# Kernel optimization log

Hardware: AMD Instinct MI355X
Metric: run time of the kernel (lower is better)

The kernel has to match this reference:

```python
import jax, jax.numpy as jnp
import numpy as np

LAM = 0.43
IN_DIM = 256
BATCH = 512


def _persistence_pairs(D):
    """0-dim persistence pairs via Kruskal-style union-find (matches torch code).
    D: [n, n] numpy distance matrix. Returns [n-1, 2] int array of MST edges."""
    n = D.shape[0]
    parent = np.arange(n)

    def find(u):
        root = u
        while parent[root] != root:
            root = parent[root]
        while parent[u] != root:  # path compression
            parent[u], u = root, parent[u]
        return root

    iu, ju = np.triu_indices(n)  # includes diagonal, like triu_indices_from
    w = D[iu, ju]
    order = np.argsort(w, kind='stable')
    pairs = []
    for e in order:
        u, v = int(iu[e]), int(ju[e])
        ru, rv = find(u), find(v)
        if ru == rv:
            continue
        if ru > rv:
            parent[rv] = ru  # merge(v, u)
        else:
            parent[ru] = rv  # merge(u, v)
        pairs.append((u, v) if u < v else (v, u))
    return np.asarray(pairs, dtype=np.int64)  # exactly n-1 edges


def _pdist(x):
    # torch.norm(x[:, None] - x, dim=2, p=2)
    return jnp.linalg.norm(x[:, None, :] - x[None, :, :], axis=-1)


def setup_inputs() -> dict:
    key = jax.random.key(0)
    ks = jax.random.split(key, 16)
    d = IN_DIM
    dims = [(d, d // 2), (d // 2, d // 4), (d // 4, 2), (2, d // 4), (d // 4, d // 2), (d // 2, d)]
    inp = {
        'x': jax.random.normal(ks[0], (BATCH, d), dtype=jnp.float32),
        'label': jax.random.randint(ks[1], (BATCH,), 0, 10),
    }
    names = ['1', '2', 'm', '3', '4', '5']
    for i, (nm, (din, dout)) in enumerate(zip(names, dims)):
        s = 1.0 / np.sqrt(din)
        inp['W' + nm] = jax.random.uniform(ks[2 + 2 * i], (din, dout), minval=-s, maxval=s, dtype=jnp.float32)
        inp['b' + nm] = jax.random.uniform(ks[3 + 2 * i], (dout,), minval=-s, maxval=s, dtype=jnp.float32)
    inp['latent_norm'] = jnp.ones((1,), dtype=jnp.float32)
    return inp


def reference(x, label, W1, b1, W2, b2, Wm, bm, W3, b3, W4, b4, W5, b5, latent_norm):
    # Encoder
    h1 = jax.nn.relu(x @ W1 + b1)
    h2 = jax.nn.relu(h1 @ W2 + b2)
    lat = h2 @ Wm + bm  # [B, 2]

    # normalized pairwise distance matrices
    xd = _pdist(x)
    xd = xd / xd.max()  # 2D-input branch
    ld = _pdist(lat) / latent_norm[0]

    # Decoder
    h3 = jax.nn.relu(lat @ W3 + b3)
    h4 = jax.nn.relu(h3 @ W4 + b4)
    xr = h4 @ W5 + b5
    ae_loss = jnp.mean((x - xr) ** 2)

    # persistence pairs (detached / host computation, as in the torch code)
    p1 = _persistence_pairs(np.asarray(jax.device_get(xd)))
    p2 = _persistence_pairs(np.asarray(jax.device_get(ld)))

    sig1 = xd[p1[:, 0], p1[:, 1]]
    sig1_2 = ld[p1[:, 0], p1[:, 1]]
    sig2 = ld[p2[:, 0], p2[:, 1]]
    sig2_1 = xd[p2[:, 0], p2[:, 1]]
    topo = jnp.sum((sig1 - sig1_2) ** 2) + jnp.sum((sig2 - sig2_1) ** 2)

    loss = ae_loss + LAM * topo / float(x.shape[0])
    return loss
```

## Files before the change

kernel.cpp:

```cpp
#include <hip/hip_runtime.h>
#include <math.h>

#define N      512
#define DIN    256
#define LAM    0.43f
#define MAGIC  0x4D535431u
#define PAD(j) ((j) + (((j) >> 6) << 2))

#define OFF_LDREADY 4
#define OFF_T0READY 5
#define OFF_T0BITS  6
#define OFF_BLKMAX  8
#define OFF_AEPART  128
#define OFF_LAT     1024
#define OFF_XD      2048
#define OFF_LD      (2048 + 262144)
#define OFF_CAND    526336
#define OFF_BAR     (OFF_CAND + 18432)

__device__ __forceinline__ unsigned ld_acq(unsigned* p) {
    return __hip_atomic_load(p, __ATOMIC_ACQUIRE, __HIP_MEMORY_SCOPE_AGENT);
}
__device__ __forceinline__ void st_rel(unsigned* p, unsigned v) {
    __hip_atomic_store(p, v, __ATOMIC_RELEASE, __HIP_MEMORY_SCOPE_AGENT);
}
__device__ __forceinline__ unsigned ld_rlx(unsigned* p) {
    return __hip_atomic_load(p, __ATOMIC_RELAXED, __HIP_MEMORY_SCOPE_AGENT);
}
__device__ __forceinline__ unsigned long long ld64_rlx(unsigned long long* p) {
    return __hip_atomic_load(p, __ATOMIC_RELAXED, __HIP_MEMORY_SCOPE_AGENT);
}
__device__ __forceinline__ void st64_rlx(unsigned long long* p, unsigned long long v) {
    __hip_atomic_store(p, v, __ATOMIC_RELAXED, __HIP_MEMORY_SCOPE_AGENT);
}
__device__ __forceinline__ void spin_magic(unsigned* p) {
    while (ld_acq(p) != MAGIC) __builtin_amdgcn_s_sleep(1);
}

__global__ __launch_bounds__(256) void fused_mlp_pdistx_kernel(
    const float* __restrict__ x,
    const float* __restrict__ W1, const float* __restrict__ b1,
    const float* __restrict__ W2, const float* __restrict__ b2,
    const float* __restrict__ Wm, const float* __restrict__ bm,
    const float* __restrict__ W3, const float* __restrict__ b3,
    const float* __restrict__ W4, const float* __restrict__ b4,
    const float* __restrict__ W5, const float* __restrict__ b5,
    float* __restrict__ lat_out, float* __restrict__ ae_part,
    float* __restrict__ xd, float* __restrict__ blkmax)
{
    const int tid = threadIdx.x;

    if (blockIdx.x < 512) {
        __shared__ float xs[256];
        __shared__ float h1[128];
        __shared__ float h2[64];
        __shared__ float latv[2];
        __shared__ float h3[64];
        __shared__ float h4[128];
        __shared__ float red[4];

        const int row = blockIdx.x;
        xs[tid] = x[(size_t)row * DIN + tid];
        __syncthreads();

        if (tid < 128) {
            float s = b1[tid];
            for (int k = 0; k < 256; ++k) s = fmaf(xs[k], W1[k * 128 + tid], s);
            h1[tid] = fmaxf(s, 0.f);
        }
        __syncthreads();

        if (tid < 64) {
            float s = b2[tid];
            for (int k = 0; k < 128; ++k) s = fmaf(h1[k], W2[k * 64 + tid], s);
            h2[tid] = fmaxf(s, 0.f);
        }
        __syncthreads();

        if (tid < 2) {
            float s = bm[tid];
            for (int k = 0; k < 64; ++k) s = fmaf(h2[k], Wm[k * 2 + tid], s);
            latv[tid] = s;
            lat_out[(size_t)row * 2 + tid] = s;
        }
        __syncthreads();

        if (tid < 64) {
            float s = b3[tid];
            s = fmaf(latv[0], W3[tid], s);
            s = fmaf(latv[1], W3[64 + tid], s);
            h3[tid] = fmaxf(s, 0.f);
        }
        __syncthreads();

        if (tid < 128) {
            float s = b4[tid];
            for (int k = 0; k < 64; ++k) s = fmaf(h3[k], W4[k * 128 + tid], s);
            h4[tid] = fmaxf(s, 0.f);
        }
        __syncthreads();

        float s = b5[tid];
        for (int k = 0; k < 128; ++k) s = fmaf(h4[k], W5[k * 256 + tid], s);
        float diff = xs[tid] - s;
        float a = diff * diff;

        #pragma unroll
        for (int m = 1; m < 64; m <<= 1) a += __shfl_xor(a, m, 64);
        if ((tid & 63) == 0) red[tid >> 6] = a;
        __syncthreads();
        if (tid == 0) ae_part[row] = red[0] + red[1] + red[2] + red[3];
    } else {
        __shared__ float As[32][65];
        __shared__ float Bs[32][65];
        __shared__ float red2[4];

        const int bid = blockIdx.x - 512;
        const int bi = bid & 7, bj = bid >> 3;
        const int i0 = bi * 64, j0 = bj * 64;
        const int ty = tid >> 4, tx = tid & 15;

        float acc[4][4];
        #pragma unroll
        for (int i = 0; i < 4; ++i)
            #pragma unroll
            for (int j = 0; j < 4; ++j) acc[i][j] = 0.f;

        for (int kk = 0; kk < DIN; kk += 32) {
            #pragma unroll
            for (int s = tid; s < 512; s += 256) {
                int r = s >> 3, c4 = (s & 7) << 2;
                float4 va = *(const float4*)(x + (size_t)(i0 + r) * DIN + kk + c4);
                As[c4 + 0][r] = va.x; As[c4 + 1][r] = va.y;
                As[c4 + 2][r] = va.z; As[c4 + 3][r] = va.w;
                float4 vb = *(const float4*)(x + (size_t)(j0 + r) * DIN + kk + c4);
                Bs[c4 + 0][r] = vb.x; Bs[c4 + 1][r] = vb.y;
                Bs[c4 + 2][r] = vb.z; Bs[c4 + 3][r] = vb.w;
            }
            __syncthreads();
            #pragma unroll 8
            for (int k = 0; k < 32; ++k) {
                float a[4], b[4];
                #pragma unroll
                for (int i = 0; i < 4; ++i) a[i] = As[k][ty + 16 * i];
                #pragma unroll
                for (int j = 0; j < 4; ++j) b[j] = Bs[k][tx + 16 * j];
                #pragma unroll
                for (int i = 0; i < 4; ++i)
                    #pragma unroll
                    for (int j = 0; j < 4; ++j) {
                        float d = a[i] - b[j];
                        acc[i][j] = fmaf(d, d, acc[i][j]);
                    }
            }
            __syncthreads();
        }

        float lmax = 0.f;
        #pragma unroll
        for (int i = 0; i < 4; ++i)
            #pragma unroll
            for (int j = 0; j < 4; ++j) {
                float dd = sqrtf(acc[i][j]);
                int r = i0 + ty + 16 * i, c = j0 + tx + 16 * j;
                xd[(size_t)r * N + c] = dd;
                lmax = fmaxf(lmax, dd);
            }

        #pragma unroll
        for (int m = 32; m >= 1; m >>= 1) lmax = fmaxf(lmax, __shfl_xor(lmax, m, 64));
        if ((tid & 63) == 0) red2[tid >> 6] = lmax;
        __syncthreads();
        if (tid == 0)
            blkmax[bid] = fmaxf(fmaxf(red2[0], red2[1]), fmaxf(red2[2], red2[3]));
    }
}

__global__ __launch_bounds__(256) void mst_boruvka_kernel(
    const float* __restrict__ xd, float* __restrict__ ld,
    const float* __restrict__ lat, const float* __restrict__ latent_norm,
    const float* __restrict__ blkmax, const float* __restrict__ ae_part,
    float* __restrict__ wsf, float* __restrict__ out)
{
    __shared__ unsigned comp_a[512];
    __shared__ __align__(16) unsigned comp_s[544];
    __shared__ unsigned long long cval[512];
    __shared__ int tgt[512];
    __shared__ unsigned short eu[512], ev[512];
    __shared__ float ew[512];
    __shared__ float latx[512], laty[512];
    __shared__ float s_red[4];
    __shared__ float s_xdm;
    __shared__ int s_ecnt;

    const int tid = threadIdx.x;
    const int blk = blockIdx.x;
    const int m   = blk >> 6;
    const int wb  = blk & 63;
    const bool leader = (wb == 0);

    unsigned* ldready = (unsigned*)(wsf + OFF_LDREADY);
    unsigned* t0ready = (unsigned*)(wsf + OFF_T0READY);
    unsigned* t0bits  = (unsigned*)(wsf + OFF_T0BITS);
    unsigned long long* candm =
        (unsigned long long*)(wsf + OFF_CAND) + (size_t)m * 9 * 512;
    unsigned* bar = (unsigned*)(wsf + OFF_BAR) + (size_t)m * 640;

    const float* Dm = m ? ld : xd;
    const float* Om = m ? xd : ld;

    if (m == 1) {
        for (int i = tid; i < 512; i += 256) {
            latx[i] = lat[2 * i + 0];
            laty[i] = lat[2 * i + 1];
        }
        __syncthreads();
        const int r0 = wb << 3;
        for (int q = tid; q < 1024; q += 256) {
            int rr = r0 + (q >> 7);
            int j  = (q & 127) << 2;
            float xi = latx[rr], yi = laty[rr];
            float dx0 = xi - latx[j + 0], dy0 = yi - laty[j + 0];
            float dx1 = xi - latx[j + 1], dy1 = yi - laty[j + 1];
            float dx2 = xi - latx[j + 2], dy2 = yi - laty[j + 2];
            float dx3 = xi - latx[j + 3], dy3 = yi - laty[j + 3];
            float4 o;
            o.x = sqrtf(fmaf(dx0, dx0, dy0 * dy0));
            o.y = sqrtf(fmaf(dx1, dx1, dy1 * dy1));
            o.z = sqrtf(fmaf(dx2, dx2, dy2 * dy2));
            o.w = sqrtf(fmaf(dx3, dx3, dy3 * dy3));
            *(float4*)(ld + (size_t)rr * N + j) = o;
        }
    }

    for (int i = tid; i < 72; i += 256)
        st64_rlx(&candm[(size_t)wb * 72 + i], ~0ULL);

    for (int i = tid; i < 512; i += 256) {
        comp_a[i] = (unsigned)i;
        comp_s[PAD(i)] = (unsigned)i;
    }
    if (tid == 0) s_ecnt = 0;

    __syncthreads();
    if (tid == 0) st_rel(&bar[wb], MAGIC);
    if (tid < 64) spin_magic(&bar[tid]);
    __syncthreads();
    if (m == 1 && leader && tid == 0) st_rel(ldready, MAGIC);

    int nc = 512;
    for (int p = 0; p < 9 && nc > 1; ++p) {
        unsigned long long* cand = candm + (size_t)p * 512;

        {
            const int r  = (wb << 3) + (tid >> 5);
            const int c0 = (tid & 31) << 4;
            const unsigned cv = comp_s[PAD(r)];
            const float4* rp = (const float4*)(Dm + (size_t)r * N + c0);
            unsigned long long bk = ~0ULL;
            #pragma unroll
            for (int c = 0; c < 4; ++c) {
                float4 f = rp[c];
                int jb = c0 + 4 * c;
                int4 cc = *(const int4*)&comp_s[PAD(jb)];
                unsigned long long k;
                k = ((unsigned long long)__float_as_uint(f.x) << 18)
                  | ((unsigned long long)r << 9) | (unsigned)(jb + 0);
                if ((unsigned)cc.x != cv && k < bk) bk = k;
                k = ((unsigned long long)__float_as_uint(f.y) << 18)
                  | ((unsigned long long)r << 9) | (unsigned)(jb + 1);
                if ((unsigned)cc.y != cv && k < bk) bk = k;
                k = ((unsigned long long)__float_as_uint(f.z) << 18)
                  | ((unsigned long long)r << 9) | (unsigned)(jb + 2);
                if ((unsigned)cc.z != cv && k < bk) bk = k;
                k = ((unsigned long long)__float_as_uint(f.w) << 18)
                  | ((unsigned long long)r << 9) | (unsigned)(jb + 3);
                if ((unsigned)cc.w != cv && k < bk) bk = k;
            }
            #pragma unroll
            for (int mm = 1; mm <= 16; mm <<= 1) {
                unsigned long long o = __shfl_xor(bk, mm, 64);
                if (o < bk) bk = o;
            }
            if ((tid & 31) == 0 && bk != ~0ULL)
                atomicMin(&cand[cv], bk);
        }

        __syncthreads();
        if (tid == 0) st_rel(&bar[(p + 1) * 64 + wb], MAGIC);
        if (tid < 64) spin_magic(&bar[(p + 1) * 64 + tid]);
        __syncthreads();

        for (int i = tid; i < 512; i += 256) cval[i] = ld64_rlx(&cand[i]);
        __syncthreads();
        for (int i = tid; i < 512; i += 256) {
            int t = -1;
            if (comp_a[i] == (unsigned)i && cval[i] != ~0ULL)
                t = (int)comp_a[cval[i] & 511];
            tgt[i] = t;
        }
        __syncthreads();
        for (int i = tid; i < 512; i += 256) {
            int s = tgt[i];
            if (s >= 0 && !(tgt[s] == i && i > s)) {
                comp_a[i] = (unsigned)s;
                int e = atomicAdd(&s_ecnt, 1);
                unsigned long long c = cval[i];
                eu[e] = (unsigned short)((c >> 9) & 511);
                ev[e] = (unsigned short)(c & 511);
                ew[e] = __uint_as_float((unsigned)(c >> 18));
            }
        }
        __syncthreads();
        for (int dd = 0; dd < 9; ++dd) {
            unsigned a = comp_a[comp_a[tid]];
            unsigned b = comp_a[comp_a[tid + 256]];
            __syncthreads();
            comp_a[tid] = a; comp_a[tid + 256] = b;
            __syncthreads();
        }
        for (int i = tid; i < 512; i += 256) comp_s[PAD(i)] = comp_a[i];
        nc = 512 - s_ecnt;
        __syncthreads();
    }

    if (!leader) return;

    if (tid < 64) {
        float mx = blkmax[tid];
        #pragma unroll
        for (int mm = 32; mm >= 1; mm >>= 1)
            mx = fmaxf(mx, __shfl_xor(mx, mm, 64));
        if (tid == 0) s_xdm = mx;
    }
    __syncthreads();
    const float xdm = s_xdm;
    const float lnv = latent_norm[0];
    const float sD = (m == 0) ? 1.f / xdm : 1.f / lnv;
    const float sO = (m == 0) ? 1.f / lnv : 1.f / xdm;

    if (m == 0) {
        if (tid == 0) spin_magic(ldready);
        __syncthreads();
    }

    const int ne = s_ecnt;
    float acc = 0.f;
    for (int i = tid; i < ne; i += 256) {
        float de = ew[i];
        float oe = Om[(size_t)eu[i] * N + ev[i]];
        float c = sD * de - sO * oe;
        acc = fmaf(c, c, acc);
    }
    #pragma unroll
    for (int mm = 32; mm >= 1; mm >>= 1) acc += __shfl_xor(acc, mm, 64);
    if ((tid & 63) == 0) s_red[tid >> 6] = acc;
    __syncthreads();

    if (m == 0) {
        if (tid == 0) {
            float t0 = s_red[0] + s_red[1] + s_red[2] + s_red[3];
            __hip_atomic_store(t0bits, __float_as_uint(t0), __ATOMIC_RELAXED,
                               __HIP_MEMORY_SCOPE_AGENT);
            st_rel(t0ready, MAGIC);
        }
    } else {
        float t1 = 0.f;
        if (tid == 0) t1 = s_red[0] + s_red[1] + s_red[2] + s_red[3];
        __syncthreads();
        float a = ae_part[tid] + ae_part[tid + 256];
        #pragma unroll
        for (int mm = 32; mm >= 1; mm >>= 1) a += __shfl_xor(a, mm, 64);
        if ((tid & 63) == 0) s_red[tid >> 6] = a;
        __syncthreads();
        if (tid == 0) {
            float ae = s_red[0] + s_red[1] + s_red[2] + s_red[3];
            spin_magic(t0ready);
            float t0 = __uint_as_float(ld_rlx(t0bits));
            out[0] = ae * (1.f / (float)(N * DIN))
                   + (LAM * (t0 + t1)) * (1.f / (float)N);
        }
    }
}

extern "C" void kernel_launch(void* const* d_in, const int* in_sizes, int n_in,
                              void* d_out, int out_size, void* d_ws, size_t ws_size,
                              hipStream_t stream) {
    const float* x   = (const float*)d_in[0];
    const float* W1  = (const float*)d_in[2];
    const float* b1  = (const float*)d_in[3];
    const float* W2  = (const float*)d_in[4];
    const float* b2  = (const float*)d_in[5];
    const float* Wm  = (const float*)d_in[6];
    const float* bm  = (const float*)d_in[7];
    const float* W3  = (const float*)d_in[8];
    const float* b3  = (const float*)d_in[9];
    const float* W4  = (const float*)d_in[10];
    const float* b4  = (const float*)d_in[11];
    const float* W5  = (const float*)d_in[12];
    const float* b5  = (const float*)d_in[13];
    const float* latent_norm = (const float*)d_in[14];

    float* ws      = (float*)d_ws;
    float* blkmax  = ws + OFF_BLKMAX;
    float* ae_part = ws + OFF_AEPART;
    float* lat     = ws + OFF_LAT;
    float* xd      = ws + OFF_XD;
    float* ld      = ws + OFF_LD;

    fused_mlp_pdistx_kernel<<<576, 256, 0, stream>>>(
        x, W1, b1, W2, b2, Wm, bm, W3, b3, W4, b4, W5, b5,
        lat, ae_part, xd, blkmax);
    mst_boruvka_kernel<<<128, 256, 0, stream>>>(
        xd, ld, lat, latent_norm, blkmax, ae_part, ws, (float*)d_out);
}
```

Baseline: 159.2 us.

## Merge MLP, pdist and Boruvka MST into one persistent 128-block kernel

Fuses both launches into a single 128-block kernel. Group 0 computes the x distance matrix and group 1 runs the autoencoder eight rows per block, with the weight loads reused across rows. Groups coordinate through global spin barriers instead of a kernel boundary. Distributed Boruvka rounds now stop once 64 components remain, after which a leader block finishes the MST on a 64x64 component table held in shared memory, trading global barriers for single-block work. This drops one launch and several cross-block barrier rounds, but adds more shared memory per block and relies on all 128 blocks being co-resident.

```diff
diff --git a/kernel.cpp b/kernel.cpp
--- a/kernel.cpp
+++ b/kernel.cpp
@@ -1,5 +1,7 @@
 #include <hip/hip_runtime.h>
 #include <math.h>
+
+typedef unsigned long long ull;
 
 #define N      512
 #define DIN    256
@@ -10,13 +12,15 @@
 #define OFF_LDREADY 4
 #define OFF_T0READY 5
 #define OFF_T0BITS  6
+#define OFF_XDREADY 7
 #define OFF_BLKMAX  8
 #define OFF_AEPART  128
 #define OFF_LAT     1024
 #define OFF_XD      2048
 #define OFF_LD      (2048 + 262144)
 #define OFF_CAND    526336
-#define OFF_BAR     (OFF_CAND + 18432)
+#define OFF_PTAB    (OFF_CAND + 6144)
+#define OFF_BAR     (OFF_PTAB + 16384)
 
 __device__ __forceinline__ unsigned ld_acq(unsigned* p) {
     return __hip_atomic_load(p, __ATOMIC_ACQUIRE, __HIP_MEMORY_SCOPE_AGENT);
@@ -27,17 +31,17 @@
 __device__ __forceinline__ unsigned ld_rlx(unsigned* p) {
     return __hip_atomic_load(p, __ATOMIC_RELAXED, __HIP_MEMORY_SCOPE_AGENT);
 }
-__device__ __forceinline__ unsigned long long ld64_rlx(unsigned long long* p) {
+__device__ __forceinline__ ull ld64_rlx(ull* p) {
     return __hip_atomic_load(p, __ATOMIC_RELAXED, __HIP_MEMORY_SCOPE_AGENT);
 }
-__device__ __forceinline__ void st64_rlx(unsigned long long* p, unsigned long long v) {
+__device__ __forceinline__ void st64_rlx(ull* p, ull v) {
     __hip_atomic_store(p, v, __ATOMIC_RELAXED, __HIP_MEMORY_SCOPE_AGENT);
 }
 __device__ __forceinline__ void spin_magic(unsigned* p) {
     while (ld_acq(p) != MAGIC) __builtin_amdgcn_s_sleep(1);
 }
 
-__global__ __launch_bounds__(256) void fused_mlp_pdistx_kernel(
+__global__ __launch_bounds__(256) void mega_kernel(
     const float* __restrict__ x,
     const float* __restrict__ W1, const float* __restrict__ b1,
     const float* __restrict__ W2, const float* __restrict__ b2,
@@ -45,78 +49,61 @@
     const float* __restrict__ W3, const float* __restrict__ b3,
     const float* __restrict__ W4, const float* __restrict__ b4,
     const float* __restrict__ W5, const float* __restrict__ b5,
-    float* __restrict__ lat_out, float* __restrict__ ae_part,
-    float* __restrict__ xd, float* __restrict__ blkmax)
+    const float* __restrict__ latent_norm,
+    float* __restrict__ wsf, float* __restrict__ out)
 {
+    __shared__ __align__(16) unsigned char scratch[32768];
+    __shared__ unsigned comp_a[512];
+    __shared__ __align__(16) unsigned comp_s[544];
+    __shared__ ull cval[512];
+    __shared__ int tgt[512];
+    __shared__ unsigned short eu[512], ev[512];
+    __shared__ float ew[512];
+    __shared__ float latx[512], laty[512];
+    __shared__ float latv[8][2];
+    __shared__ float aered[4][8];
+    __shared__ int s_arow[8];
+    __shared__ unsigned lc[64];
+    __shared__ int lt_[64];
+    __shared__ ull rcn[64];
+    __shared__ float s_red[4];
+    __shared__ float s_xdm;
+    __shared__ int s_ecnt, s_h;
+
     const int tid = threadIdx.x;
-
-    if (blockIdx.x < 512) {
-        __shared__ float xs[256];
-        __shared__ float h1[128];
-        __shared__ float h2[64];
-        __shared__ float latv[2];
-        __shared__ float h3[64];
-        __shared__ float h4[128];
-        __shared__ float red[4];
-
-        const int row = blockIdx.x;
-        xs[tid] = x[(size_t)row * DIN + tid];
-        __syncthreads();
-
-        if (tid < 128) {
-            float s = b1[tid];
-            for (int k = 0; k < 256; ++k) s = fmaf(xs[k], W1[k * 128 + tid], s);
-            h1[tid] = fmaxf(s, 0.f);
-        }
-        __syncthreads();
-
-        if (tid < 64) {
-            float s = b2[tid];
-            for (int k = 0; k < 128; ++k) s = fmaf(h1[k], W2[k * 64 + tid], s);
-            h2[tid] = fmaxf(s, 0.f);
-        }
-        __syncthreads();
-
-        if (tid < 2) {
-            float s = bm[tid];
-            for (int k = 0; k < 64; ++k) s = fmaf(h2[k], Wm[k * 2 + tid], s);
-            latv[tid] = s;
-            lat_out[(size_t)row * 2 + tid] = s;
-        }
-        __syncthreads();
-
-        if (tid < 64) {
-            float s = b3[tid];
-            s = fmaf(latv[0], W3[tid], s);
-            s = fmaf(latv[1], W3[64 + tid], s);
-            h3[tid] = fmaxf(s, 0.f);
-        }
-        __syncthreads();
-
-        if (tid < 128) {
-            float s = b4[tid];
-            for (int k = 0; k < 64; ++k) s = fmaf(h3[k], W4[k * 128 + tid], s);
-            h4[tid] = fmaxf(s, 0.f);
-        }
-        __syncthreads();
-
-        float s = b5[tid];
-        for (int k = 0; k < 128; ++k) s = fmaf(h4[k], W5[k * 256 + tid], s);
-        float diff = xs[tid] - s;
-        float a = diff * diff;
-
-        #pragma unroll
-        for (int m = 1; m < 64; m <<= 1) a += __shfl_xor(a, m, 64);
-        if ((tid & 63) == 0) red[tid >> 6] = a;
-        __syncthreads();
-        if (tid == 0) ae_part[row] = red[0] + red[1] + red[2] + red[3];
-    } else {
-        __shared__ float As[32][65];
-        __shared__ float Bs[32][65];
-        __shared__ float red2[4];
-
-        const int bid = blockIdx.x - 512;
-        const int bi = bid & 7, bj = bid >> 3;
+    const int blk = blockIdx.x;
+    const int m   = blk >> 6;
+    const int wb  = blk & 63;
+    const bool leader = (wb == 0);
+    const float INF = __int_as_float(0x7f800000);
+
+    float* xd     = wsf + OFF_XD;
+    float* ld     = wsf + OFF_LD;
+    float* latg   = wsf + OFF_LAT;
+    float* blkmax = wsf + OFF_BLKMAX;
+    float* ae_g   = wsf + OFF_AEPART;
+    unsigned* ldready = (unsigned*)(wsf + OFF_LDREADY);
+    unsigned* t0ready = (unsigned*)(wsf + OFF_T0READY);
+    unsigned* t0bits  = (unsigned*)(wsf + OFF_T0BITS);
+    unsigned* xdready = (unsigned*)(wsf + OFF_XDREADY);
+    ull* candm = (ull*)(wsf + OFF_CAND) + (size_t)m * 1536;
+    ull* ptabm = (ull*)(wsf + OFF_PTAB) + (size_t)m * 4096;
+    unsigned* barw = (unsigned*)(wsf + OFF_BAR);
+    unsigned* xbar = barw;
+    unsigned* mbar = barw + 64;
+    unsigned* lbar = barw + 128;
+    unsigned* pbar = barw + 192 + (size_t)m * 256;
+
+    const float* Dm = m ? ld : xd;
+    const float* Om = m ? xd : ld;
+
+    for (int i = tid; i < 24; i += 256) st64_rlx(&candm[(size_t)wb * 24 + i], ~0ULL);
+    for (int i = tid; i < 64; i += 256) st64_rlx(&ptabm[(size_t)wb * 64 + i], ~0ULL);
+
+    if (m == 0) {
+        float (*As)[65] = (float(*)[65])scratch;
+        float (*Bs)[65] = (float(*)[65])(scratch + 8320);
+        const int bi = wb & 7, bj = wb >> 3;
         const int i0 = bi * 64, j0 = bj * 64;
         const int ty = tid >> 4, tx = tid & 15;
 
@@ -166,56 +153,130 @@
                 xd[(size_t)r * N + c] = dd;
                 lmax = fmaxf(lmax, dd);
             }
-
         #pragma unroll
-        for (int m = 32; m >= 1; m >>= 1) lmax = fmaxf(lmax, __shfl_xor(lmax, m, 64));
-        if ((tid & 63) == 0) red2[tid >> 6] = lmax;
+        for (int mm = 32; mm >= 1; mm >>= 1) lmax = fmaxf(lmax, __shfl_xor(lmax, mm, 64));
+        if ((tid & 63) == 0) s_red[tid >> 6] = lmax;
         __syncthreads();
         if (tid == 0)
-            blkmax[bid] = fmaxf(fmaxf(red2[0], red2[1]), fmaxf(red2[2], red2[3]));
-    }
-}
-
-__global__ __launch_bounds__(256) void mst_boruvka_kernel(
-    const float* __restrict__ xd, float* __restrict__ ld,
-    const float* __restrict__ lat, const float* __restrict__ latent_norm,
-    const float* __restrict__ blkmax, const float* __restrict__ ae_part,
-    float* __restrict__ wsf, float* __restrict__ out)
-{
-    __shared__ unsigned comp_a[512];
-    __shared__ __align__(16) unsigned comp_s[544];
-    __shared__ unsigned long long cval[512];
-    __shared__ int tgt[512];
-    __shared__ unsigned short eu[512], ev[512];
-    __shared__ float ew[512];
-    __shared__ float latx[512], laty[512];
-    __shared__ float s_red[4];
-    __shared__ float s_xdm;
-    __shared__ int s_ecnt;
-
-    const int tid = threadIdx.x;
-    const int blk = blockIdx.x;
-    const int m   = blk >> 6;
-    const int wb  = blk & 63;
-    const bool leader = (wb == 0);
-
-    unsigned* ldready = (unsigned*)(wsf + OFF_LDREADY);
-    unsigned* t0ready = (unsigned*)(wsf + OFF_T0READY);
-    unsigned* t0bits  = (unsigned*)(wsf + OFF_T0BITS);
-    unsigned long long* candm =
-        (unsigned long long*)(wsf + OFF_CAND) + (size_t)m * 9 * 512;
-    unsigned* bar = (unsigned*)(wsf + OFF_BAR) + (size_t)m * 640;
-
-    const float* Dm = m ? ld : xd;
-    const float* Om = m ? xd : ld;
-
-    if (m == 1) {
+            blkmax[wb] = fmaxf(fmaxf(s_red[0], s_red[1]), fmaxf(s_red[2], s_red[3]));
+        __syncthreads();
+        if (tid == 0) st_rel(&xbar[wb], MAGIC);
+        if (tid < 64) spin_magic(&xbar[tid]);
+        __syncthreads();
+        if (leader && tid == 0) st_rel(xdready, MAGIC);
+    } else {
+        float* xs = (float*)scratch;
+        float* h1 = xs + 2048;
+        float* h2 = h1 + 1024;
+        float* h3 = h2 + 512;
+        float* h4 = h3 + 512;
+        const int r0 = wb << 3;
+
+        for (int q = tid; q < 512; q += 256) {
+            int rr = q >> 6, c4 = (q & 63) << 2;
+            *(float4*)&xs[rr * 256 + c4] =
+                *(const float4*)(x + (size_t)(r0 + rr) * DIN + c4);
+        }
+        __syncthreads();
+        {
+            int c = tid & 127, rb = (tid >> 7) << 2;
+            float a0 = b1[c], a1 = a0, a2 = a0, a3 = a0;
+            #pragma unroll 4
+            for (int k = 0; k < 256; ++k) {
+                float w = W1[k * 128 + c];
+                a0 = fmaf(xs[(rb + 0) * 256 + k], w, a0);
+                a1 = fmaf(xs[(rb + 1) * 256 + k], w, a1);
+                a2 = fmaf(xs[(rb + 2) * 256 + k], w, a2);
+                a3 = fmaf(xs[(rb + 3) * 256 + k], w, a3);
+            }
+            h1[(rb + 0) * 128 + c] = fmaxf(a0, 0.f);
+            h1[(rb + 1) * 128 + c] = fmaxf(a1, 0.f);
+            h1[(rb + 2) * 128 + c] = fmaxf(a2, 0.f);
+            h1[(rb + 3) * 128 + c] = fmaxf(a3, 0.f);
+        }
+        __syncthreads();
+        {
+            int c = tid & 63, rb = (tid >> 6) << 1;
+            float a0 = b2[c], a1 = a0;
+            #pragma unroll 4
+            for (int k = 0; k < 128; ++k) {
+                float w = W2[k * 64 + c];
+                a0 = fmaf(h1[(rb + 0) * 128 + k], w, a0);
+                a1 = fmaf(h1[(rb + 1) * 128 + k], w, a1);
+            }
+            h2[(rb + 0) * 64 + c] = fmaxf(a0, 0.f);
+            h2[(rb + 1) * 64 + c] = fmaxf(a1, 0.f);
+        }
+        __syncthreads();
+        if (tid < 16) {
+            int r = tid >> 1, c = tid & 1;
+            float a = bm[c];
+            #pragma unroll 4
+            for (int k = 0; k < 64; ++k) a = fmaf(h2[r * 64 + k], Wm[k * 2 + c], a);
+            latv[r][c] = a;
+            latg[(size_t)(r0 + r) * 2 + c] = a;
+        }
+        __syncthreads();
+        {
+            int c = tid & 63, rb = (tid >> 6) << 1;
+            #pragma unroll
+            for (int j = 0; j < 2; ++j) {
+                int r = rb + j;
+                float a = b3[c] + latv[r][0] * W3[c] + latv[r][1] * W3[64 + c];
+                h3[r * 64 + c] = fmaxf(a, 0.f);
+            }
+        }
+        __syncthreads();
+        {
+            int c = tid & 127, rb = (tid >> 7) << 2;
+            float a0 = b4[c], a1 = a0, a2 = a0, a3 = a0;
+            #pragma unroll 4
+            for (int k = 0; k < 64; ++k) {
+                float w = W4[k * 128 + c];
+                a0 = fmaf(h3[(rb + 0) * 64 + k], w, a0);
+                a1 = fmaf(h3[(rb + 1) * 64 + k], w, a1);
+                a2 = fmaf(h3[(rb + 2) * 64 + k], w, a2);
+                a3 = fmaf(h3[(rb + 3) * 64 + k], w, a3);
+            }
+            h4[(rb + 0) * 128 + c] = fmaxf(a0, 0.f);
+            h4[(rb + 1) * 128 + c] = fmaxf(a1, 0.f);
+            h4[(rb + 2) * 128 + c] = fmaxf(a2, 0.f);
+            h4[(rb + 3) * 128 + c] = fmaxf(a3, 0.f);
+        }
+        __syncthreads();
+        {
+            int c = tid;
+            float a[8];
+            #pragma unroll
+            for (int r = 0; r < 8; ++r) a[r] = b5[c];
+            #pragma unroll 2
+            for (int k = 0; k < 128; ++k) {
+                float w = W5[k * 256 + c];
+                #pragma unroll
+                for (int r = 0; r < 8; ++r) a[r] = fmaf(h4[r * 128 + k], w, a[r]);
+            }
+            #pragma unroll
+            for (int r = 0; r < 8; ++r) {
+                float d = xs[r * 256 + c] - a[r];
+                float v = d * d;
+                #pragma unroll
+                for (int mm = 1; mm < 64; mm <<= 1) v += __shfl_xor(v, mm, 64);
+                if ((tid & 63) == 0) aered[tid >> 6][r] = v;
+            }
+            __syncthreads();
+            if (tid < 8)
+                ae_g[r0 + tid] = aered[0][tid] + aered[1][tid]
+                               + aered[2][tid] + aered[3][tid];
+        }
+        __syncthreads();
+        if (tid == 0) st_rel(&mbar[wb], MAGIC);
+        if (tid < 64) spin_magic(&mbar[tid]);
+        __syncthreads();
         for (int i = tid; i < 512; i += 256) {
-            latx[i] = lat[2 * i + 0];
-            laty[i] = lat[2 * i + 1];
-        }
-        __syncthreads();
-        const int r0 = wb << 3;
+            float2 v = *(const float2*)(latg + 2 * i);
+            latx[i] = v.x; laty[i] = v.y;
+        }
+        __syncthreads();
         for (int q = tid; q < 1024; q += 256) {
             int rr = r0 + (q >> 7);
             int j  = (q & 127) << 2;
@@ -231,64 +292,54 @@
             o.w = sqrtf(fmaf(dx3, dx3, dy3 * dy3));
             *(float4*)(ld + (size_t)rr * N + j) = o;
         }
-    }
-
-    for (int i = tid; i < 72; i += 256)
-        st64_rlx(&candm[(size_t)wb * 72 + i], ~0ULL);
+        __syncthreads();
+        if (tid == 0) st_rel(&lbar[wb], MAGIC);
+        if (tid < 64) spin_magic(&lbar[tid]);
+        __syncthreads();
+        if (leader && tid == 0) st_rel(ldready, MAGIC);
+    }
 
     for (int i = tid; i < 512; i += 256) {
         comp_a[i] = (unsigned)i;
         comp_s[PAD(i)] = (unsigned)i;
     }
     if (tid == 0) s_ecnt = 0;
-
     __syncthreads();
-    if (tid == 0) st_rel(&bar[wb], MAGIC);
-    if (tid < 64) spin_magic(&bar[tid]);
-    __syncthreads();
-    if (m == 1 && leader && tid == 0) st_rel(ldready, MAGIC);
-
-    int nc = 512;
-    for (int p = 0; p < 9 && nc > 1; ++p) {
-        unsigned long long* cand = candm + (size_t)p * 512;
-
+
+    int nc = 512, p = 0;
+    while (nc > 64) {
+        ull* cand = candm + (size_t)p * 512;
         {
             const int r  = (wb << 3) + (tid >> 5);
             const int c0 = (tid & 31) << 4;
             const unsigned cv = comp_s[PAD(r)];
             const float4* rp = (const float4*)(Dm + (size_t)r * N + c0);
-            unsigned long long bk = ~0ULL;
+            ull bk = ~0ULL;
             #pragma unroll
             for (int c = 0; c < 4; ++c) {
                 float4 f = rp[c];
                 int jb = c0 + 4 * c;
                 int4 cc = *(const int4*)&comp_s[PAD(jb)];
-                unsigned long long k;
-                k = ((unsigned long long)__float_as_uint(f.x) << 18)
-                  | ((unsigned long long)r << 9) | (unsigned)(jb + 0);
+                ull k;
+                k = ((ull)__float_as_uint(f.x) << 18) | ((ull)r << 9) | (unsigned)(jb + 0);
                 if ((unsigned)cc.x != cv && k < bk) bk = k;
-                k = ((unsigned long long)__float_as_uint(f.y) << 18)
-                  | ((unsigned long long)r << 9) | (unsigned)(jb + 1);
+                k = ((ull)__float_as_uint(f.y) << 18) | ((ull)r << 9) | (unsigned)(jb + 1);
                 if ((unsigned)cc.y != cv && k < bk) bk = k;
-                k = ((unsigned long long)__float_as_uint(f.z) << 18)
-                  | ((unsigned long long)r << 9) | (unsigned)(jb + 2);
+                k = ((ull)__float_as_uint(f.z) << 18) | ((ull)r << 9) | (unsigned)(jb + 2);
                 if ((unsigned)cc.z != cv && k < bk) bk = k;
-                k = ((unsigned long long)__float_as_uint(f.w) << 18)
-                  | ((unsigned long long)r << 9) | (unsigned)(jb + 3);
+                k = ((ull)__float_as_uint(f.w) << 18) | ((ull)r << 9) | (unsigned)(jb + 3);
                 if ((unsigned)cc.w != cv && k < bk) bk = k;
             }
             #pragma unroll
             for (int mm = 1; mm <= 16; mm <<= 1) {
-                unsigned long long o = __shfl_xor(bk, mm, 64);
+                ull o = __shfl_xor(bk, mm, 64);
                 if (o < bk) bk = o;
             }
-            if ((tid & 31) == 0 && bk != ~0ULL)
-                atomicMin(&cand[cv], bk);
-        }
-
-        __syncthreads();
-        if (tid == 0) st_rel(&bar[(p + 1) * 64 + wb], MAGIC);
-        if (tid < 64) spin_magic(&bar[(p + 1) * 64 + tid]);
+            if ((tid & 31) == 0 && bk != ~0ULL) atomicMin(&cand[cv], bk);
+        }
+        __syncthreads();
+        if (tid == 0) st_rel(&pbar[p * 64 + wb], MAGIC);
+        if (tid < 64) spin_magic(&pbar[p * 64 + tid]);
         __syncthreads();
 
         for (int i = tid; i < 512; i += 256) cval[i] = ld64_rlx(&cand[i]);
@@ -305,7 +356,7 @@
             if (s >= 0 && !(tgt[s] == i && i > s)) {
                 comp_a[i] = (unsigned)s;
                 int e = atomicAdd(&s_ecnt, 1);
-                unsigned long long c = cval[i];
+                ull c = cval[i];
                 eu[e] = (unsigned short)((c >> 9) & 511);
                 ev[e] = (unsigned short)(c & 511);
                 ew[e] = __uint_as_float((unsigned)(c >> 18));
@@ -322,15 +373,133 @@
         for (int i = tid; i < 512; i += 256) comp_s[PAD(i)] = comp_a[i];
         nc = 512 - s_ecnt;
         __syncthreads();
-    }
-
-    if (!leader) return;
+        ++p;
+    }
+
+    if (nc > 1) {
+        if (tid < 64) {
+            int base = tid << 3;
+            unsigned f[8]; unsigned cnt = 0;
+            #pragma unroll
+            for (int k = 0; k < 8; ++k) {
+                f[k] = (comp_a[base + k] == (unsigned)(base + k)) ? 1u : 0u;
+                cnt += f[k];
+            }
+            unsigned s = cnt;
+            #pragma unroll
+            for (int o = 1; o < 64; o <<= 1) {
+                unsigned v = __shfl_up(s, o, 64);
+                if (tid >= o) s += v;
+            }
+            int run = (int)(s - cnt);
+            #pragma unroll
+            for (int k = 0; k < 8; ++k)
+                if (f[k]) tgt[base + k] = run++;
+        }
+        __syncthreads();
+
+        ull* rowT = cval;
+        for (int i = tid; i < 512; i += 256) rowT[i] = ~0ULL;
+        if (tid < 8) s_arow[tid] = tgt[comp_a[(wb << 3) + tid]];
+        __syncthreads();
+        {
+            const int rl = tid >> 5;
+            const int r  = (wb << 3) + rl;
+            const int c0 = (tid & 31) << 4;
+            const int av = tgt[comp_a[r]];
+            const float4* rp = (const float4*)(Dm + (size_t)r * N + c0);
+            #pragma unroll
+            for (int c = 0; c < 4; ++c) {
+                float4 f = rp[c];
+                int jb = c0 + 4 * c;
+                const float w4[4] = {f.x, f.y, f.z, f.w};
+                #pragma unroll
+                for (int t4 = 0; t4 < 4; ++t4) {
+                    int j = jb + t4;
+                    int b = tgt[comp_a[j]];
+                    if (b != av) {
+                        ull k = ((ull)__float_as_uint(w4[t4]) << 18)
+                              | ((ull)r << 9) | (unsigned)j;
+                        atomicMin(&rowT[rl * 64 + b], k);
+                    }
+                }
+            }
+        }
+        __syncthreads();
+        for (int i = tid; i < 512; i += 256) {
+            ull v = rowT[i];
+            if (v != ~0ULL)
+                atomicMin(&ptabm[(size_t)s_arow[i >> 6] * 64 + (i & 63)], v);
+        }
+        __syncthreads();
+        if (tid == 0) st_rel(&pbar[p * 64 + wb], MAGIC);
+        if (!leader) return;
+        if (tid < 64) spin_magic(&pbar[p * 64 + tid]);
+        __syncthreads();
+
+        ull* ptabL = (ull*)scratch;
+        for (int i = tid; i < 4096; i += 256) ptabL[i] = ld64_rlx(&ptabm[i]);
+        if (tid < 64) lc[tid] = (unsigned)tid;
+        __syncthreads();
+        int lnc = nc;
+        for (int round = 0; round < 6 && lnc > 1; ++round) {
+            if (tid < 64) rcn[tid] = ~0ULL;
+            __syncthreads();
+            if (tid < nc) {
+                unsigned la = lc[tid];
+                ull bk = ~0ULL;
+                for (int b = 0; b < nc; ++b) {
+                    if (lc[b] != la) {
+                        ull k = ptabL[tid * 64 + b];
+                        if (k < bk) bk = k;
+                    }
+                }
+                if (bk != ~0ULL) atomicMin(&rcn[la], bk);
+            }
+            __syncthreads();
+            if (tid < 64) {
+                int t = -1;
+                if (tid < nc && lc[tid] == (unsigned)tid && rcn[tid] != ~0ULL) {
+                    int jv = (int)(rcn[tid] & 511);
+                    t = (int)lc[tgt[comp_a[jv]]];
+                }
+                lt_[tid] = t;
+            }
+            if (tid == 0) s_h = 0;
+            __syncthreads();
+            if (tid < 64) {
+                int t = lt_[tid];
+                if (t >= 0 && !(lt_[t] == tid && tid > t)) {
+                    lc[tid] = (unsigned)t;
+                    int e = atomicAdd(&s_ecnt, 1);
+                    atomicAdd(&s_h, 1);
+                    ull k = rcn[tid];
+                    eu[e] = (unsigned short)((k >> 9) & 511);
+                    ev[e] = (unsigned short)(k & 511);
+                    ew[e] = __uint_as_float((unsigned)(k >> 18));
+                }
+            }
+            __syncthreads();
+            for (int dd = 0; dd < 6; ++dd) {
+                unsigned v = (tid < 64) ? lc[lc[tid]] : 0u;
+                __syncthreads();
+                if (tid < 64) lc[tid] = v;
+                __syncthreads();
+            }
+            lnc -= s_h;
+            __syncthreads();
+        }
+    } else {
+        if (!leader) return;
+    }
+
+    if (m == 1) { if (tid == 0) spin_magic(xdready); __syncthreads(); }
+    else        { if (tid == 0) spin_magic(ldready); __syncthreads(); }
 
     if (tid < 64) {
         float mx = blkmax[tid];
         #pragma unroll
-        for (int mm = 32; mm >= 1; mm >>= 1)
-            mx = fmaxf(mx, __shfl_xor(mx, mm, 64));
+        for (int mm = 32; mm >= 1; mm >>= 1) mx = fmaxf(mx, __shfl_xor(mx, mm, 64));
         if (tid == 0) s_xdm = mx;
     }
     __syncthreads();
@@ -338,11 +507,6 @@
     const float lnv = latent_norm[0];
     const float sD = (m == 0) ? 1.f / xdm : 1.f / lnv;
     const float sO = (m == 0) ? 1.f / lnv : 1.f / xdm;
-
-    if (m == 0) {
-        if (tid == 0) spin_magic(ldready);
-        __syncthreads();
-    }
 
     const int ne = s_ecnt;
     float acc = 0.f;
@@ -368,7 +532,7 @@
         float t1 = 0.f;
         if (tid == 0) t1 = s_red[0] + s_red[1] + s_red[2] + s_red[3];
         __syncthreads();
-        float a = ae_part[tid] + ae_part[tid + 256];
+        float a = ae_g[tid] + ae_g[tid + 256];
         #pragma unroll
         for (int mm = 32; mm >= 1; mm >>= 1) a += __shfl_xor(a, mm, 64);
         if ((tid & 63) == 0) s_red[tid >> 6] = a;
@@ -386,6 +550,7 @@
 extern "C" void kernel_launch(void* const* d_in, const int* in_sizes, int n_in,
                               void* d_out, int out_size, void* d_ws, size_t ws_size,
                               hipStream_t stream) {
+    (void)in_sizes; (void)n_in; (void)out_size; (void)ws_size;
     const float* x   = (const float*)d_in[0];
     const float* W1  = (const float*)d_in[2];
     const float* b1  = (const float*)d_in[3];
@@ -401,16 +566,7 @@
     const float* b5  = (const float*)d_in[13];
     const float* latent_norm = (const float*)d_in[14];
 
-    float* ws      = (float*)d_ws;
-    float* blkmax  = ws + OFF_BLKMAX;
-    float* ae_part = ws + OFF_AEPART;
-    float* lat     = ws + OFF_LAT;
-    float* xd      = ws + OFF_XD;
-    float* ld      = ws + OFF_LD;
-
-    fused_mlp_pdistx_kernel<<<576, 256, 0, stream>>>(
+    mega_kernel<<<128, 256, 0, stream>>>(
         x, W1, b1, W2, b2, Wm, bm, W3, b3, W4, b4, W5, b5,
-        lat, ae_part, xd, blkmax);
-    mst_boruvka_kernel<<<128, 256, 0, stream>>>(
-        xd, ld, lat, latent_norm, blkmax, ae_part, ws, (float*)d_out);
-}
+        latent_norm, (float*)d_ws, (float*)d_out);
+}
```

New measurement: 183.6 us. 15.3% more time.
